# Optimization experiments

Measured on AMD Instinct MI355X. Metric: run time of the kernel, lower is better.

## Reference

```python
import jax, jax.numpy as jnp
import numpy as np

B = 16384      # batch
N = 128        # number of DNPU nodes (experts)
I = 3          # data electrodes per node
C = 4          # control electrodes per node
E = I + C      # total electrodes = 7
H = 90         # surrogate-model hidden width
L = 3          # number of extra hidden layers


def setup_inputs() -> dict:
    key = jax.random.key(0)
    ks = jax.random.split(key, 8)
    s_in = 1.0 / np.sqrt(E)
    s_h = 1.0 / np.sqrt(H)
    return {
        "x": jax.random.normal(ks[0], (B, N * I), dtype=jnp.float32),
        "controls": jax.random.uniform(ks[1], (N, C), dtype=jnp.float32, minval=-1.2, maxval=0.6),
        "W_in": jax.random.normal(ks[2], (N, E, H), dtype=jnp.float32) * s_in,
        "b_in": jax.random.normal(ks[3], (N, H), dtype=jnp.float32) * 0.1,
        "W_hid": jax.random.normal(ks[4], (L, N, H, H), dtype=jnp.float32) * s_h,
        "b_hid": jax.random.normal(ks[5], (L, N, H), dtype=jnp.float32) * 0.1,
        "W_out": jax.random.normal(ks[6], (N, H), dtype=jnp.float32) * s_h,
        "b_out": jax.random.normal(ks[7], (N,), dtype=jnp.float32) * 0.1,
    }


def reference(x, controls, W_in, b_in, W_hid, b_hid, W_out, b_out):
    # DNPU_Layer: partition x into N chunks of I, each node merges its data
    # electrodes with its learned control voltages into a 7-electrode vector,
    # evaluates the shared surrogate MLP with per-node parameters, outputs 1
    # current per node; results are concatenated along dim 1 -> [B, N].
    b = x.shape[0]
    xd = x.reshape(b, N, I)                                   # partition_input
    ctrl = jnp.broadcast_to(controls[None], (b, N, C))        # per-node controls
    e = jnp.concatenate([xd, ctrl], axis=-1)                  # [B, N, E]
    h = jax.nn.relu(jnp.einsum('bne,neh->bnh', e, W_in) + b_in)
    for l in range(L):  # fixed small layer count
        h = jax.nn.relu(jnp.einsum('bnh,nhk->bnk', h, W_hid[l]) + b_hid[l])
    out = jnp.einsum('bnh,nh->bn', h, W_out) + b_out          # [B, N]
    return out
```

## Files before the change

### kernel.cpp

```cpp
#include <hip/hip_runtime.h>
#include <stdint.h>

namespace {
constexpr int kB  = 16384;
constexpr int kN  = 128;
constexpr int kI  = 3;
constexpr int kC  = 4;
constexpr int kH  = 90;
constexpr int kL  = 3;
constexpr int KP  = 96;
constexpr int FB_PER_NODE = 57;
constexpr int NODE_USH    = FB_PER_NODE * 512;
constexpr size_t WT_BYTES = (size_t)kN * NODE_USH * 2;
constexpr size_t WO_OFF   = WT_BYTES;
constexpr size_t XK_OFF   = WO_OFF + (size_t)kN * KP * 4;
constexpr size_t OT_OFF   = XK_OFF + (size_t)kN * kI * kB * 2;
}

typedef __attribute__((ext_vector_type(8))) short bf16x8;
typedef __attribute__((ext_vector_type(4))) float f32x4;
typedef __attribute__((ext_vector_type(16))) float f32x16;

__device__ __forceinline__ uint32_t pack_bf16(float lo, float hi) {
#if __has_builtin(__builtin_amdgcn_cvt_pk_bf16_f32)
  auto r = __builtin_amdgcn_cvt_pk_bf16_f32(lo, hi);
  union { decltype(r) v; uint32_t u; } c; c.v = r; return c.u;
#else
  union { float f; uint32_t i; } a, b; a.f = lo; b.f = hi;
  uint32_t ua = a.i + 0x8000u;
  uint32_t ub = b.i + 0x8000u;
  return __builtin_amdgcn_perm(ub, ua, 0x07060302);
#endif
}
__device__ __forceinline__ ushort f2bf(float f) {
  union { float f; uint32_t i; } v; v.f = f;
  uint32_t u = v.i + 0x7FFFu + ((v.i >> 16) & 1u);
  return (ushort)(u >> 16);
}

__device__ __forceinline__ void pl32swap(uint32_t& a, uint32_t& b) {
#if __has_builtin(__builtin_amdgcn_permlane32_swap)
  auto r = __builtin_amdgcn_permlane32_swap(a, b, false, false);
  a = (uint32_t)r[0]; b = (uint32_t)r[1];
#else
  uint32_t sa = (uint32_t)__shfl_xor((int)a, 32);
  uint32_t sb = (uint32_t)__shfl_xor((int)b, 32);
  bool lo = (threadIdx.x & 63) < 32;
  uint32_t na = lo ? a : sb;
  uint32_t nb = lo ? sa : b;
  a = na; b = nb;
#endif
}

__device__ __forceinline__ void stage16(const ushort* g, ushort* l) {
  __builtin_amdgcn_global_load_lds(
      (const __attribute__((address_space(1))) void*)g,
      (__attribute__((address_space(3))) void*)l, 16, 0, 0);
}

__global__ __launch_bounds__(256) void prep_kernel(
    const float* __restrict__ x,
    const float* __restrict__ W_in, const float* __restrict__ b_in,
    const float* __restrict__ W_hid, const float* __restrict__ b_hid,
    const float* __restrict__ W_out, const float* __restrict__ b_out,
    ushort* __restrict__ wt, float* __restrict__ wo, ushort* __restrict__ xk)
{
  __shared__ float smem[kH * (kH + 1) + kH];
  const int tid = threadIdx.x;
  const int bid = blockIdx.x;

  if (bid < 4 * kN) {
    float* ldsw = smem;
    float* ldsb = smem + kH * (kH + 1);
    const int node  = bid & (kN - 1);
    const int layer = bid >> 7;
    const int ksrc  = (layer == 0) ? (kI + kC) : kH;
    const float* src;
    const float* bsrc;
    if (layer == 0) { src = W_in + (size_t)node * (kI + kC) * kH; bsrc = b_in + (size_t)node * kH; }
    else {
      int l = layer - 1;
      src  = W_hid + (size_t)(l * kN + node) * kH * kH;
      bsrc = b_hid + (size_t)(l * kN + node) * kH;
    }
    for (int idx = tid; idx < ksrc * kH; idx += 256)
      ldsw[(idx / kH) * (kH + 1) + (idx % kH)] = src[idx];
    if (tid < kH) ldsb[tid] = bsrc[tid];
    __syncthreads();
    ushort* dstbase = wt + (size_t)node * NODE_USH
                    + (size_t)((layer == 0) ? 0 : 3 + (layer - 1) * 18) * 512;
    const int nch = (layer == 0) ? 192 : 1152;
#pragma unroll
    for (int it = 0; it < 5; ++it) {
      int c = tid + it * 256;
      if (c < nch) {
        int fb = c >> 6, lane = c & 63;
        int ks = (layer == 0) ? 0 : fb / 3;
        int mt = (layer == 0) ? fb : fb % 3;
        int j  = mt * 32 + (lane & 31);
        int kb = ks * 16 + (lane >> 5) * 8;
        float v[8];
#pragma unroll
        for (int i = 0; i < 8; ++i) {
          int k = kb + i;
          float t = 0.f;
          if (j < kH) {
            if (k < ksrc)       t = ldsw[k * (kH + 1) + j];
            else if (k == ksrc) t = ldsb[j];
          }
          v[i] = t;
        }
        uint4 p;
        p.x = pack_bf16(v[0], v[1]); p.y = pack_bf16(v[2], v[3]);
        p.z = pack_bf16(v[4], v[5]); p.w = pack_bf16(v[6], v[7]);
        *(uint4*)&dstbase[(size_t)c * 8] = p;
      }
    }
  } else if (bid < 4 * kN + 4) {
    int base = (bid - 4 * kN) * 3072;
    for (int t = 0; t < 12; ++t) {
      int idx = base + t * 256 + tid;
      int node = idx / KP, j = idx % KP;
      float v = 0.f;
      if (j < kH)       v = W_out[node * kH + j];
      else if (j == kH) v = b_out[node];
      wo[idx] = v;
    }
  } else {
    int xb = bid - (4 * kN + 4);
    int b0 = (xb & 255) * 64;
    int c0 = (xb >> 8) * 96;
    float* lds = smem;
    for (int idx = tid; idx < 64 * 96; idx += 256) {
      int r = idx / 96, c = idx % 96;
      lds[r * 97 + c] = x[(size_t)(b0 + r) * (kN * kI) + c0 + c];
    }
    __syncthreads();
#pragma unroll
    for (int it = 0; it < 3; ++it) {
      int c = tid + it * 256;
      int nk = c >> 3, b = (c & 7) * 8;
      float v[8];
#pragma unroll
      for (int i = 0; i < 8; ++i) v[i] = lds[(b + i) * 97 + nk];
      uint4 p;
      p.x = pack_bf16(v[0], v[1]); p.y = pack_bf16(v[2], v[3]);
      p.z = pack_bf16(v[4], v[5]); p.w = pack_bf16(v[6], v[7]);
      *(uint4*)&xk[(size_t)(c0 + nk) * kB + b0 + b] = p;
    }
  }
}

__global__ __launch_bounds__(256, 3) void dnpu_kernel(
    const ushort* __restrict__ xk, const float* __restrict__ controls,
    const ushort* __restrict__ wt, const float* __restrict__ wo,
    float* __restrict__ outT)
{
  __shared__ __align__(16) ushort wbuf[2][18 * 512];

  const int tid  = threadIdx.x;
  const int lane = tid & 63;
  const int wid  = tid >> 6;
  const int node = (int)(blockIdx.x & 127);
  const int m0   = (int)(blockIdx.x >> 7) * 256 + wid * 64;
  const int col  = lane & 31;
  const int hh   = lane >> 5;

  const ushort* wnode = wt + (size_t)node * NODE_USH;

  auto stage_hid = [&](int l, ushort* buf) {
    const ushort* src = wnode + (size_t)(3 + l * 18) * 512;
#pragma unroll
    for (int r = 0; r < 4; ++r)
      stage16(src + (size_t)(r * 256 + wid * 64 + lane) * 8,
              buf + (size_t)(r * 256 + wid * 64) * 8);
    if (wid < 2)
      stage16(src + (size_t)(1024 + wid * 64 + lane) * 8,
              buf + (size_t)(1024 + wid * 64) * 8);
  };

  if (wid < 3)
    stage16(wnode + (size_t)(wid * 64 + lane) * 8, &wbuf[0][(size_t)(wid * 64) * 8]);
  stage_hid(0, &wbuf[1][0]);

  const f32x16 zf = (f32x16)0.0f;
  f32x16 acc[3][2];

  bf16x8 b0[2];
  {
    const ushort cb0 = f2bf(controls[node * kC + 0]);
    const ushort cb1 = f2bf(controls[node * kC + 1]);
    const ushort cb2 = f2bf(controls[node * kC + 2]);
    const ushort cb3 = f2bf(controls[node * kC + 3]);
    const ushort* xp = xk + (size_t)node * kI * kB + m0 + col;
#pragma unroll
    for (int nt = 0; nt < 2; ++nt) {
      union { ushort s[8]; bf16x8 v; } f;
      f.s[0] = xp[0 * kB + nt * 32];
      f.s[1] = xp[1 * kB + nt * 32];
      f.s[2] = xp[2 * kB + nt * 32];
      f.s[3] = cb0; f.s[4] = cb1; f.s[5] = cb2; f.s[6] = cb3;
      f.s[7] = 0x3F80;
      bf16x8 z = (bf16x8){0,0,0,0,0,0,0,0};
      if (hh) b0[nt] = z; else b0[nt] = f.v;
    }
  }

  union BF { uint32_t u[4]; bf16x8 v; };
  BF Bw[6][2];

  auto packB = [&]() {
#pragma unroll
    for (int mt = 0; mt < 3; ++mt)
#pragma unroll
      for (int nt = 0; nt < 2; ++nt) {
        float v[16];
#pragma unroll
        for (int r = 0; r < 16; ++r) v[r] = fmaxf(acc[mt][nt][r], 0.f);
        if (mt == 2) v[14] = (hh == 0) ? 1.0f : v[14];
        uint32_t P[8];
#pragma unroll
        for (int w = 0; w < 8; ++w) P[w] = pack_bf16(v[2 * w], v[2 * w + 1]);
        uint32_t a0 = P[0], c0 = P[2]; pl32swap(a0, c0);
        uint32_t a1 = P[1], c1 = P[3]; pl32swap(a1, c1);
        uint32_t a2 = P[4], c2 = P[6]; pl32swap(a2, c2);
        uint32_t a3 = P[5], c3 = P[7]; pl32swap(a3, c3);
        Bw[2 * mt][nt].u[0] = a0; Bw[2 * mt][nt].u[1] = a1;
        Bw[2 * mt][nt].u[2] = c0; Bw[2 * mt][nt].u[3] = c1;
        Bw[2 * mt + 1][nt].u[0] = a2; Bw[2 * mt + 1][nt].u[1] = a3;
        Bw[2 * mt + 1][nt].u[2] = c2; Bw[2 * mt + 1][nt].u[3] = c3;
      }
  };

  auto compute_hidden = [&](const ushort* buf) {
    __builtin_amdgcn_s_setprio(1);
#pragma unroll
    for (int ks = 0; ks < 6; ++ks)
#pragma unroll
      for (int mt = 0; mt < 3; ++mt) {
        bf16x8 afr = *(const bf16x8*)&buf[(size_t)(ks * 3 + mt) * 512 + lane * 8];
#pragma unroll
        for (int nt = 0; nt < 2; ++nt)
          acc[mt][nt] = __builtin_amdgcn_mfma_f32_32x32x16_bf16(
              afr, Bw[ks][nt].v, (ks == 0) ? zf : acc[mt][nt], 0, 0, 0);
      }
    __builtin_amdgcn_s_setprio(0);
  };

  __syncthreads();

  {
    __builtin_amdgcn_s_setprio(1);
#pragma unroll
    for (int mt = 0; mt < 3; ++mt) {
      bf16x8 afr = *(const bf16x8*)&wbuf[0][(size_t)mt * 512 + lane * 8];
#pragma unroll
      for (int nt = 0; nt < 2; ++nt)
        acc[mt][nt] = __builtin_amdgcn_mfma_f32_32x32x16_bf16(afr, b0[nt], zf, 0, 0, 0);
    }
    __builtin_amdgcn_s_setprio(0);
  }

  packB();
  __syncthreads();
  stage_hid(1, &wbuf[0][0]);
  compute_hidden(&wbuf[1][0]);

  packB();
  __syncthreads();
  stage_hid(2, &wbuf[1][0]);
  compute_hidden(&wbuf[0][0]);

  packB();
  __syncthreads();
  compute_hidden(&wbuf[1][0]);

  {
    const float* wop = wo + node * KP;
    float s0 = 0.f, s1 = 0.f;
#pragma unroll
    for (int mt = 0; mt < 3; ++mt) {
#pragma unroll
      for (int g = 0; g < 4; ++g) {
        float4 wf = *(const float4*)&wop[mt * 32 + g * 8 + hh * 4];
#pragma unroll
        for (int r2 = 0; r2 < 4; ++r2) {
          int r = g * 4 + r2;
          float w = (r2 == 0) ? wf.x : (r2 == 1) ? wf.y : (r2 == 2) ? wf.z : wf.w;
          float h0v = fmaxf(acc[mt][0][r], 0.f);
          float h1v = fmaxf(acc[mt][1][r], 0.f);
          if (mt == 2 && r == 14) {
            h0v = (hh == 0) ? 1.0f : h0v;
            h1v = (hh == 0) ? 1.0f : h1v;
          }
          s0 += h0v * w; s1 += h1v * w;
        }
      }
    }
    s0 += __shfl_xor(s0, 32);
    s1 += __shfl_xor(s1, 32);
    float r = hh ? s1 : s0;
    outT[(size_t)node * kB + m0 + lane] = r;
  }
}

__global__ __launch_bounds__(256) void transpose_out(
    const float* __restrict__ ot, float* __restrict__ out)
{
  __shared__ float t[64][65];
  const int b0 = (int)(blockIdx.x & 255) * 64;
  const int n0 = (int)(blockIdx.x >> 8) * 64;
  const int c  = threadIdx.x & 63;
  const int r4 = threadIdx.x >> 6;
#pragma unroll
  for (int i = 0; i < 16; ++i) {
    int n = r4 + i * 4;
    t[n][c] = ot[(size_t)(n0 + n) * kB + b0 + c];
  }
  __syncthreads();
#pragma unroll
  for (int i = 0; i < 16; ++i) {
    int b = r4 + i * 4;
    out[(size_t)(b0 + b) * kN + n0 + c] = t[c][b];
  }
}

extern "C" void kernel_launch(void* const* d_in, const int* in_sizes, int n_in,
                              void* d_out, int out_size, void* d_ws, size_t ws_size,
                              hipStream_t stream) {
  const float* x        = (const float*)d_in[0];
  const float* controls = (const float*)d_in[1];
  const float* W_in     = (const float*)d_in[2];
  const float* b_in     = (const float*)d_in[3];
  const float* W_hid    = (const float*)d_in[4];
  const float* b_hid    = (const float*)d_in[5];
  const float* W_out    = (const float*)d_in[6];
  const float* b_out    = (const float*)d_in[7];
  float* out = (float*)d_out;

  ushort* wt = (ushort*)d_ws;
  float*  wo = (float*)((char*)d_ws + WO_OFF);
  ushort* xk = (ushort*)((char*)d_ws + XK_OFF);
  float*  ot = (float*)((char*)d_ws + OT_OFF);

  hipLaunchKernelGGL(prep_kernel, dim3(4 * kN + 4 + 1024), dim3(256), 0, stream,
                     x, W_in, b_in, W_hid, b_hid, W_out, b_out, wt, wo, xk);

  dim3 grid((kB / 256) * kN);
  hipLaunchKernelGGL(dnpu_kernel, grid, dim3(256), 0, stream,
                     xk, controls, wt, wo, ot);

  hipLaunchKernelGGL(transpose_out, dim3(512), dim3(256), 0, stream, ot, out);
}
```

Measured before the change: 219.7 us.

## Read x directly in main kernel and write output untransposed, dropping transposes

Removes the x transpose/bf16 conversion stage from the prep kernel and the separate output transpose kernel. The main kernel now reads fp32 x straight from its original [B, N*I] layout, converting to bf16 in registers, and writes results directly into the [B, N] output. This saves two intermediate global round-trips and one kernel launch. In exchange, the x reads and output stores are strided: each lane touches a different row, with a 1536-byte stride for x and 512 bytes for the output, so coalescing is poor.

```diff
diff --git a/kernel.cpp b/kernel.cpp
--- a/kernel.cpp
+++ b/kernel.cpp
@@ -13,8 +13,6 @@
 constexpr int NODE_USH    = FB_PER_NODE * 512;
 constexpr size_t WT_BYTES = (size_t)kN * NODE_USH * 2;
 constexpr size_t WO_OFF   = WT_BYTES;
-constexpr size_t XK_OFF   = WO_OFF + (size_t)kN * KP * 4;
-constexpr size_t OT_OFF   = XK_OFF + (size_t)kN * kI * kB * 2;
 }
 
 typedef __attribute__((ext_vector_type(8))) short bf16x8;
@@ -59,11 +57,10 @@
 }
 
 __global__ __launch_bounds__(256) void prep_kernel(
-    const float* __restrict__ x,
     const float* __restrict__ W_in, const float* __restrict__ b_in,
     const float* __restrict__ W_hid, const float* __restrict__ b_hid,
     const float* __restrict__ W_out, const float* __restrict__ b_out,
-    ushort* __restrict__ wt, float* __restrict__ wo, ushort* __restrict__ xk)
+    ushort* __restrict__ wt, float* __restrict__ wo)
 {
   __shared__ float smem[kH * (kH + 1) + kH];
   const int tid = threadIdx.x;
@@ -116,7 +113,7 @@
         *(uint4*)&dstbase[(size_t)c * 8] = p;
       }
     }
-  } else if (bid < 4 * kN + 4) {
+  } else {
     int base = (bid - 4 * kN) * 3072;
     for (int t = 0; t < 12; ++t) {
       int idx = base + t * 256 + tid;
@@ -126,35 +123,13 @@
       else if (j == kH) v = b_out[node];
       wo[idx] = v;
     }
-  } else {
-    int xb = bid - (4 * kN + 4);
-    int b0 = (xb & 255) * 64;
-    int c0 = (xb >> 8) * 96;
-    float* lds = smem;
-    for (int idx = tid; idx < 64 * 96; idx += 256) {
-      int r = idx / 96, c = idx % 96;
-      lds[r * 97 + c] = x[(size_t)(b0 + r) * (kN * kI) + c0 + c];
-    }
-    __syncthreads();
-#pragma unroll
-    for (int it = 0; it < 3; ++it) {
-      int c = tid + it * 256;
-      int nk = c >> 3, b = (c & 7) * 8;
-      float v[8];
-#pragma unroll
-      for (int i = 0; i < 8; ++i) v[i] = lds[(b + i) * 97 + nk];
-      uint4 p;
-      p.x = pack_bf16(v[0], v[1]); p.y = pack_bf16(v[2], v[3]);
-      p.z = pack_bf16(v[4], v[5]); p.w = pack_bf16(v[6], v[7]);
-      *(uint4*)&xk[(size_t)(c0 + nk) * kB + b0 + b] = p;
-    }
   }
 }
 
 __global__ __launch_bounds__(256, 3) void dnpu_kernel(
-    const ushort* __restrict__ xk, const float* __restrict__ controls,
+    const float* __restrict__ x, const float* __restrict__ controls,
     const ushort* __restrict__ wt, const float* __restrict__ wo,
-    float* __restrict__ outT)
+    float* __restrict__ out)
 {
   __shared__ __align__(16) ushort wbuf[2][18 * 512];
 
@@ -192,13 +167,14 @@
     const ushort cb1 = f2bf(controls[node * kC + 1]);
     const ushort cb2 = f2bf(controls[node * kC + 2]);
     const ushort cb3 = f2bf(controls[node * kC + 3]);
-    const ushort* xp = xk + (size_t)node * kI * kB + m0 + col;
+    const float* xp = x + (size_t)(m0 + col) * (kN * kI) + node * kI;
 #pragma unroll
     for (int nt = 0; nt < 2; ++nt) {
+      const float* xr = xp + (size_t)nt * 32 * (kN * kI);
       union { ushort s[8]; bf16x8 v; } f;
-      f.s[0] = xp[0 * kB + nt * 32];
-      f.s[1] = xp[1 * kB + nt * 32];
-      f.s[2] = xp[2 * kB + nt * 32];
+      f.s[0] = f2bf(xr[0]);
+      f.s[1] = f2bf(xr[1]);
+      f.s[2] = f2bf(xr[2]);
       f.s[3] = cb0; f.s[4] = cb1; f.s[5] = cb2; f.s[6] = cb3;
       f.s[7] = 0x3F80;
       bf16x8 z = (bf16x8){0,0,0,0,0,0,0,0};
@@ -300,28 +276,7 @@
     s0 += __shfl_xor(s0, 32);
     s1 += __shfl_xor(s1, 32);
     float r = hh ? s1 : s0;
-    outT[(size_t)node * kB + m0 + lane] = r;
-  }
-}
-
-__global__ __launch_bounds__(256) void transpose_out(
-    const float* __restrict__ ot, float* __restrict__ out)
-{
-  __shared__ float t[64][65];
-  const int b0 = (int)(blockIdx.x & 255) * 64;
-  const int n0 = (int)(blockIdx.x >> 8) * 64;
-  const int c  = threadIdx.x & 63;
-  const int r4 = threadIdx.x >> 6;
-#pragma unroll
-  for (int i = 0; i < 16; ++i) {
-    int n = r4 + i * 4;
-    t[n][c] = ot[(size_t)(n0 + n) * kB + b0 + c];
-  }
-  __syncthreads();
-#pragma unroll
-  for (int i = 0; i < 16; ++i) {
-    int b = r4 + i * 4;
-    out[(size_t)(b0 + b) * kN + n0 + c] = t[c][b];
+    out[(size_t)(m0 + lane) * kN + node] = r;
   }
 }
 
@@ -340,15 +295,11 @@
 
   ushort* wt = (ushort*)d_ws;
   float*  wo = (float*)((char*)d_ws + WO_OFF);
-  ushort* xk = (ushort*)((char*)d_ws + XK_OFF);
-  float*  ot = (float*)((char*)d_ws + OT_OFF);
-
-  hipLaunchKernelGGL(prep_kernel, dim3(4 * kN + 4 + 1024), dim3(256), 0, stream,
-                     x, W_in, b_in, W_hid, b_hid, W_out, b_out, wt, wo, xk);
+
+  hipLaunchKernelGGL(prep_kernel, dim3(4 * kN + 4), dim3(256), 0, stream,
+                     W_in, b_in, W_hid, b_hid, W_out, b_out, wt, wo);
 
   dim3 grid((kB / 256) * kN);
   hipLaunchKernelGGL(dnpu_kernel, grid, dim3(256), 0, stream,
-                     xk, controls, wt, wo, ot);
-
-  hipLaunchKernelGGL(transpose_out, dim3(512), dim3(256), 0, stream, ot, out);
-}
+                     x, controls, wt, wo, out);
+}
```

Measured after the change: 222.2 us. Within noise of the previous version (+1.2%).

## Fuse output transpose into main kernel and pack activations per M-tile

Applied to the files above, without the earlier changes.

Removes the separate transpose kernel and its intermediate buffer by having each thread write its node output directly to the [B,N] layout with a strided scatter store. The hidden-layer computation is restructured to finish all K steps for one M-tile before packing it into ping-pong B-operand registers, instead of holding all six accumulators until the layer ends. This lowers live accumulator register pressure and lets the pack work overlap with later MFMAs, but it needs two B-fragment register sets, and the direct output stores are uncoalesced (stride kN floats across lanes).

```diff
diff --git a/kernel.cpp b/kernel.cpp
--- a/kernel.cpp
+++ b/kernel.cpp
@@ -14,11 +14,9 @@
 constexpr size_t WT_BYTES = (size_t)kN * NODE_USH * 2;
 constexpr size_t WO_OFF   = WT_BYTES;
 constexpr size_t XK_OFF   = WO_OFF + (size_t)kN * KP * 4;
-constexpr size_t OT_OFF   = XK_OFF + (size_t)kN * kI * kB * 2;
 }
 
 typedef __attribute__((ext_vector_type(8))) short bf16x8;
-typedef __attribute__((ext_vector_type(4))) float f32x4;
 typedef __attribute__((ext_vector_type(16))) float f32x16;
 
 __device__ __forceinline__ uint32_t pack_bf16(float lo, float hi) {
@@ -154,7 +152,7 @@
 __global__ __launch_bounds__(256, 3) void dnpu_kernel(
     const ushort* __restrict__ xk, const float* __restrict__ controls,
     const ushort* __restrict__ wt, const float* __restrict__ wo,
-    float* __restrict__ outT)
+    float* __restrict__ out)
 {
   __shared__ __align__(16) ushort wbuf[2][18 * 512];
 
@@ -184,7 +182,6 @@
   stage_hid(0, &wbuf[1][0]);
 
   const f32x16 zf = (f32x16)0.0f;
-  f32x16 acc[3][2];
 
   bf16x8 b0[2];
   {
@@ -207,79 +204,88 @@
   }
 
   union BF { uint32_t u[4]; bf16x8 v; };
-  BF Bw[6][2];
-
-  auto packB = [&]() {
-#pragma unroll
-    for (int mt = 0; mt < 3; ++mt)
-#pragma unroll
-      for (int nt = 0; nt < 2; ++nt) {
-        float v[16];
-#pragma unroll
-        for (int r = 0; r < 16; ++r) v[r] = fmaxf(acc[mt][nt][r], 0.f);
-        if (mt == 2) v[14] = (hh == 0) ? 1.0f : v[14];
-        uint32_t P[8];
-#pragma unroll
-        for (int w = 0; w < 8; ++w) P[w] = pack_bf16(v[2 * w], v[2 * w + 1]);
-        uint32_t a0 = P[0], c0 = P[2]; pl32swap(a0, c0);
-        uint32_t a1 = P[1], c1 = P[3]; pl32swap(a1, c1);
-        uint32_t a2 = P[4], c2 = P[6]; pl32swap(a2, c2);
-        uint32_t a3 = P[5], c3 = P[7]; pl32swap(a3, c3);
-        Bw[2 * mt][nt].u[0] = a0; Bw[2 * mt][nt].u[1] = a1;
-        Bw[2 * mt][nt].u[2] = c0; Bw[2 * mt][nt].u[3] = c1;
-        Bw[2 * mt + 1][nt].u[0] = a2; Bw[2 * mt + 1][nt].u[1] = a3;
-        Bw[2 * mt + 1][nt].u[2] = c2; Bw[2 * mt + 1][nt].u[3] = c3;
+  BF Bc[6][2], Bn[6][2];
+
+  auto pack_mt = [&](int mt, const f32x16& a0, const f32x16& a1, BF (&Bout)[6][2]) {
+#pragma unroll
+    for (int nt = 0; nt < 2; ++nt) {
+      const f32x16& a = nt ? a1 : a0;
+      float v[16];
+#pragma unroll
+      for (int r = 0; r < 16; ++r) v[r] = fmaxf(a[r], 0.f);
+      if (mt == 2) v[14] = (hh == 0) ? 1.0f : v[14];
+      uint32_t P[8];
+#pragma unroll
+      for (int w = 0; w < 8; ++w) P[w] = pack_bf16(v[2 * w], v[2 * w + 1]);
+      uint32_t q0 = P[0], q2 = P[2]; pl32swap(q0, q2);
+      uint32_t q1 = P[1], q3 = P[3]; pl32swap(q1, q3);
+      uint32_t q4 = P[4], q6 = P[6]; pl32swap(q4, q6);
+      uint32_t q5 = P[5], q7 = P[7]; pl32swap(q5, q7);
+      Bout[2 * mt][nt].u[0] = q0; Bout[2 * mt][nt].u[1] = q1;
+      Bout[2 * mt][nt].u[2] = q2; Bout[2 * mt][nt].u[3] = q3;
+      Bout[2 * mt + 1][nt].u[0] = q4; Bout[2 * mt + 1][nt].u[1] = q5;
+      Bout[2 * mt + 1][nt].u[2] = q6; Bout[2 * mt + 1][nt].u[3] = q7;
+    }
+  };
+
+  auto hidden = [&](const ushort* buf, BF (&Bin)[6][2], BF (&Bout)[6][2]) {
+#pragma unroll
+    for (int mt = 0; mt < 3; ++mt) {
+      f32x16 a0, a1;
+      __builtin_amdgcn_s_setprio(1);
+#pragma unroll
+      for (int ks = 0; ks < 6; ++ks) {
+        bf16x8 afr = *(const bf16x8*)&buf[(size_t)(ks * 3 + mt) * 512 + lane * 8];
+        a0 = __builtin_amdgcn_mfma_f32_32x32x16_bf16(afr, Bin[ks][0].v,
+                                                     ks ? a0 : zf, 0, 0, 0);
+        a1 = __builtin_amdgcn_mfma_f32_32x32x16_bf16(afr, Bin[ks][1].v,
+                                                     ks ? a1 : zf, 0, 0, 0);
       }
+      __builtin_amdgcn_s_setprio(0);
+      pack_mt(mt, a0, a1, Bout);
+    }
   };
 
-  auto compute_hidden = [&](const ushort* buf) {
-    __builtin_amdgcn_s_setprio(1);
-#pragma unroll
-    for (int ks = 0; ks < 6; ++ks)
-#pragma unroll
-      for (int mt = 0; mt < 3; ++mt) {
-        bf16x8 afr = *(const bf16x8*)&buf[(size_t)(ks * 3 + mt) * 512 + lane * 8];
-#pragma unroll
-        for (int nt = 0; nt < 2; ++nt)
-          acc[mt][nt] = __builtin_amdgcn_mfma_f32_32x32x16_bf16(
-              afr, Bw[ks][nt].v, (ks == 0) ? zf : acc[mt][nt], 0, 0, 0);
-      }
-    __builtin_amdgcn_s_setprio(0);
-  };
-
   __syncthreads();
 
   {
-    __builtin_amdgcn_s_setprio(1);
 #pragma unroll
     for (int mt = 0; mt < 3; ++mt) {
       bf16x8 afr = *(const bf16x8*)&wbuf[0][(size_t)mt * 512 + lane * 8];
-#pragma unroll
-      for (int nt = 0; nt < 2; ++nt)
-        acc[mt][nt] = __builtin_amdgcn_mfma_f32_32x32x16_bf16(afr, b0[nt], zf, 0, 0, 0);
-    }
-    __builtin_amdgcn_s_setprio(0);
+      __builtin_amdgcn_s_setprio(1);
+      f32x16 a0 = __builtin_amdgcn_mfma_f32_32x32x16_bf16(afr, b0[0], zf, 0, 0, 0);
+      f32x16 a1 = __builtin_amdgcn_mfma_f32_32x32x16_bf16(afr, b0[1], zf, 0, 0, 0);
+      __builtin_amdgcn_s_setprio(0);
+      pack_mt(mt, a0, a1, Bc);
+    }
   }
 
-  packB();
   __syncthreads();
   stage_hid(1, &wbuf[0][0]);
-  compute_hidden(&wbuf[1][0]);
-
-  packB();
+  hidden(&wbuf[1][0], Bc, Bn);
+
   __syncthreads();
   stage_hid(2, &wbuf[1][0]);
-  compute_hidden(&wbuf[0][0]);
-
-  packB();
+  hidden(&wbuf[0][0], Bn, Bc);
+
   __syncthreads();
-  compute_hidden(&wbuf[1][0]);
 
   {
     const float* wop = wo + node * KP;
     float s0 = 0.f, s1 = 0.f;
 #pragma unroll
     for (int mt = 0; mt < 3; ++mt) {
+      f32x16 a0, a1;
+      __builtin_amdgcn_s_setprio(1);
+#pragma unroll
+      for (int ks = 0; ks < 6; ++ks) {
+        bf16x8 afr = *(const bf16x8*)&wbuf[1][(size_t)(ks * 3 + mt) * 512 + lane * 8];
+        a0 = __builtin_amdgcn_mfma_f32_32x32x16_bf16(afr, Bc[ks][0].v,
+                                                     ks ? a0 : zf, 0, 0, 0);
+        a1 = __builtin_amdgcn_mfma_f32_32x32x16_bf16(afr, Bc[ks][1].v,
+                                                     ks ? a1 : zf, 0, 0, 0);
+      }
+      __builtin_amdgcn_s_setprio(0);
 #pragma unroll
       for (int g = 0; g < 4; ++g) {
         float4 wf = *(const float4*)&wop[mt * 32 + g * 8 + hh * 4];
@@ -287,8 +293,8 @@
         for (int r2 = 0; r2 < 4; ++r2) {
           int r = g * 4 + r2;
           float w = (r2 == 0) ? wf.x : (r2 == 1) ? wf.y : (r2 == 2) ? wf.z : wf.w;
-          float h0v = fmaxf(acc[mt][0][r], 0.f);
-          float h1v = fmaxf(acc[mt][1][r], 0.f);
+          float h0v = fmaxf(a0[r], 0.f);
+          float h1v = fmaxf(a1[r], 0.f);
           if (mt == 2 && r == 14) {
             h0v = (hh == 0) ? 1.0f : h0v;
             h1v = (hh == 0) ? 1.0f : h1v;
@@ -300,28 +306,7 @@
     s0 += __shfl_xor(s0, 32);
     s1 += __shfl_xor(s1, 32);
     float r = hh ? s1 : s0;
-    outT[(size_t)node * kB + m0 + lane] = r;
-  }
-}
-
-__global__ __launch_bounds__(256) void transpose_out(
-    const float* __restrict__ ot, float* __restrict__ out)
-{
-  __shared__ float t[64][65];
-  const int b0 = (int)(blockIdx.x & 255) * 64;
-  const int n0 = (int)(blockIdx.x >> 8) * 64;
-  const int c  = threadIdx.x & 63;
-  const int r4 = threadIdx.x >> 6;
-#pragma unroll
-  for (int i = 0; i < 16; ++i) {
-    int n = r4 + i * 4;
-    t[n][c] = ot[(size_t)(n0 + n) * kB + b0 + c];
-  }
-  __syncthreads();
-#pragma unroll
-  for (int i = 0; i < 16; ++i) {
-    int b = r4 + i * 4;
-    out[(size_t)(b0 + b) * kN + n0 + c] = t[c][b];
+    out[(size_t)(m0 + lane) * kN + node] = r;
   }
 }
 
@@ -341,14 +326,11 @@
   ushort* wt = (ushort*)d_ws;
   float*  wo = (float*)((char*)d_ws + WO_OFF);
   ushort* xk = (ushort*)((char*)d_ws + XK_OFF);
-  float*  ot = (float*)((char*)d_ws + OT_OFF);
 
   hipLaunchKernelGGL(prep_kernel, dim3(4 * kN + 4 + 1024), dim3(256), 0, stream,
                      x, W_in, b_in, W_hid, b_hid, W_out, b_out, wt, wo, xk);
 
   dim3 grid((kB / 256) * kN);
   hipLaunchKernelGGL(dnpu_kernel, grid, dim3(256), 0, stream,
-                     xk, controls, wt, wo, ot);
-
-  hipLaunchKernelGGL(transpose_out, dim3(512), dim3(256), 0, stream, ot, out);
-}
+                     xk, controls, wt, wo, out);
+}
```

New measurement: 225.3 us. 2.6% more time.
